# Kernel tuning notes

Measured on AMD Instinct MI355X. Metric: run time of the kernel, lower is better.

## Reference

```python
import jax, jax.numpy as jnp
import numpy as np

HID = 1024
NH = 16
DH = HID // NH  # 64


def _heads(x):
    # [B, S, H] -> [B, nH, S, dh]
    B, S, _ = x.shape
    return x.reshape(B, S, NH, DH).transpose(0, 2, 1, 3)


def setup_inputs() -> dict:
    key = jax.random.key(0)
    ks = jax.random.split(key, 16)
    inp = {
        "word_hidden_states": jax.random.normal(ks[0], (2, 2048, HID), jnp.float32),
        "entity_hidden_states": jax.random.normal(ks[1], (2, 256, HID), jnp.float32),
    }
    scale = 1.0 / np.sqrt(HID)
    names = ["Wq", "Wk", "Wv", "Ww2e", "We2w", "We2e"]
    for i, n in enumerate(names):
        inp[n] = jax.random.normal(ks[2 + i], (HID, HID), jnp.float32) * scale
        inp["b" + n[1:]] = jnp.zeros((HID,), jnp.float32)
    return inp


def reference(word_hidden_states, entity_hidden_states,
              Wq, bq, Wk, bk, Wv, bv,
              Ww2e, bw2e, We2w, be2w, We2e, be2e):
    word, ent = word_hidden_states, entity_hidden_states
    B, Sw, _ = word.shape
    Se = ent.shape[1]
    hs = jnp.concatenate([word, ent], axis=1)  # [B, Sw+Se, H]

    # four query types, heads: [B, nH, S*, dh]
    q_w2w = _heads(word @ Wq + bq)
    q_w2e = _heads(word @ Ww2e + bw2e)
    q_e2w = _heads(ent @ We2w + be2w)
    q_e2e = _heads(ent @ We2e + be2e)

    k = _heads(hs @ Wk + bk)
    v = _heads(hs @ Wv + bv)
    k_w, k_e = k[:, :, :Sw, :], k[:, :, Sw:, :]

    # block scores
    s_w2w = jnp.einsum("bhqd,bhkd->bhqk", q_w2w, k_w)  # [B,nH,Sw,Sw]
    s_w2e = jnp.einsum("bhqd,bhkd->bhqk", q_w2e, k_e)  # [B,nH,Sw,Se]
    s_e2w = jnp.einsum("bhqd,bhkd->bhqk", q_e2w, k_w)  # [B,nH,Se,Sw]
    s_e2e = jnp.einsum("bhqd,bhkd->bhqk", q_e2e, k_e)  # [B,nH,Se,Se]

    word_scores = jnp.concatenate([s_w2w, s_w2e], axis=3)
    ent_scores = jnp.concatenate([s_e2w, s_e2e], axis=3)
    scores = jnp.concatenate([word_scores, ent_scores], axis=2)  # [B,nH,S,S]
    scores = scores / np.sqrt(DH)

    probs = jax.nn.softmax(scores, axis=-1)  # dropout is identity in eval
    ctx = jnp.einsum("bhqk,bhkd->bhqd", probs, v)  # [B,nH,S,dh]
    ctx = ctx.transpose(0, 2, 1, 3).reshape(B, Sw + Se, HID)
    return ctx[:, :Sw, :], ctx[:, Sw:, :]
```

## Files before the change

kernel.cpp:

```cpp
#include <hip/hip_runtime.h>
#include <hip/hip_bf16.h>

typedef __attribute__((ext_vector_type(8))) short short8;
typedef __attribute__((ext_vector_type(4))) float f32x4;
typedef __attribute__((ext_vector_type(16))) float f32x16;
typedef __attribute__((ext_vector_type(4))) unsigned short u16x4;
typedef __attribute__((ext_vector_type(8))) unsigned short u16x8;
typedef __attribute__((ext_vector_type(4))) unsigned int u32x4;

__device__ __forceinline__ unsigned short f2b(float f) {
  __hip_bfloat16 h = __float2bfloat16(f);
  return __builtin_bit_cast(unsigned short, h);
}

__device__ __forceinline__ void gload_lds16(const void* g, void* l) {
  __builtin_amdgcn_global_load_lds(
      (const __attribute__((address_space(1))) unsigned int*)g,
      (__attribute__((address_space(3))) unsigned int*)l, 16, 0, 0);
}

__device__ __forceinline__ f32x16 mfma32(short8 a, short8 b, f32x16 c) {
  return __builtin_amdgcn_mfma_f32_32x32x16_bf16(a, b, c, 0, 0, 0);
}

__device__ __forceinline__ unsigned int cvtpk(float a, float b) {
  unsigned int r;
  asm("v_cvt_pk_bf16_f32 %0, %1, %2" : "=v"(r) : "v"(a), "v"(b));
  return r;
}

__global__ __launch_bounds__(256) void cvt_all(const float* __restrict__ sw,
                                               const float* __restrict__ se,
                                               unsigned short* __restrict__ dw,
                                               unsigned short* __restrict__ de) {
  int i = blockIdx.x * 256 + threadIdx.x;
  const float* s;
  unsigned short* d;
  int j;
  if (i < 524288) {
    s = sw; d = dw; j = i;
  } else {
    s = se; d = de; j = i - 524288;
    if (j >= 65536) return;
  }
  const f32x4* sp = (const f32x4*)s;
  f32x4 a = sp[2 * j];
  f32x4 b = sp[2 * j + 1];
  u16x8 o;
  o[0] = f2b(a[0]); o[1] = f2b(a[1]); o[2] = f2b(a[2]); o[3] = f2b(a[3]);
  o[4] = f2b(b[0]); o[5] = f2b(b[1]); o[6] = f2b(b[2]); o[7] = f2b(b[3]);
  ((u16x8*)d)[j] = o;
}

struct WtransParams {
  const float* w[6];
  unsigned short* wt[6];
};

__global__ __launch_bounds__(256) void wtrans(WtransParams p) {
  __shared__ float t[32][33];
  const int z = blockIdx.z;
  const float* W = p.w[z];
  unsigned short* Wt = p.wt[z];
  const int bx = blockIdx.x;
  const int by = blockIdx.y;
  const int tx = threadIdx.x, ty = threadIdx.y;
#pragma unroll
  for (int i = 0; i < 4; ++i)
    t[ty + 8 * i][tx] = W[(by * 32 + ty + 8 * i) * 1024 + bx * 32 + tx];
  __syncthreads();
#pragma unroll
  for (int i = 0; i < 4; ++i)
    Wt[(bx * 32 + ty + 8 * i) * 1024 + by * 32 + tx] = f2b(t[tx][ty + 8 * i]);
}

struct GemmJob {
  const unsigned short* Wt;
  const float* bias;
  unsigned short* out;
  int S;
  int s_off;
  int sshift;
  int trans;
  float scale;
};
struct Gemm2Params {
  const unsigned short* Aw;
  const unsigned short* Ae;
  GemmJob job[8];
};

__global__ __launch_bounds__(256) void gemm_qkv(Gemm2Params p) {
  __shared__ unsigned short smem[16384];
  unsigned short* As = smem;
  unsigned short* Bs = smem + 8192;
  const int tid = threadIdx.x;
  const int w = tid >> 6, lane = tid & 63;
  const int c = lane & 15, g = lane >> 4;
  const int z = blockIdx.z;
  const int y = blockIdx.y;
  const bool isword = y < 32;
  const GemmJob j = p.job[isword ? z : z + 4];
  const unsigned short* A = isword ? p.Aw : p.Ae;
  const long arow0 = (long)(isword ? y : y - 32) * 128;
  const unsigned short* B = j.Wt;
  const long brow0 = (long)blockIdx.x * 128;

  f32x4 acc[4][4] = {};

  for (int kt = 0; kt < 16; ++kt) {
    __syncthreads();
#pragma unroll
    for (int i = 0; i < 4; ++i) {
      int ch = i * 256 + tid;
      int row = ch >> 3;
      int k8 = ((ch & 7) ^ (row & 7)) << 3;
      const unsigned short* ga = A + (arow0 + row) * 1024 + kt * 64 + k8;
      const unsigned short* gb = B + (brow0 + row) * 1024 + kt * 64 + k8;
      gload_lds16(ga, As + (i * 256 + w * 64) * 8);
      gload_lds16(gb, Bs + (i * 256 + w * 64) * 8);
    }
    __syncthreads();
#pragma unroll
    for (int kf = 0; kf < 2; ++kf) {
      short8 av[4], bv[4];
#pragma unroll
      for (int mf = 0; mf < 4; ++mf) {
        int row = (w >> 1) * 64 + mf * 16 + c;
        int byte = (row * 128 + (kf * 32 + g * 8) * 2) ^ ((row & 7) << 4);
        av[mf] = *(const short8*)((const char*)As + byte);
      }
#pragma unroll
      for (int nf = 0; nf < 4; ++nf) {
        int row = (w & 1) * 64 + nf * 16 + c;
        int byte = (row * 128 + (kf * 32 + g * 8) * 2) ^ ((row & 7) << 4);
        bv[nf] = *(const short8*)((const char*)Bs + byte);
      }
      __builtin_amdgcn_s_setprio(1);
#pragma unroll
      for (int mf = 0; mf < 4; ++mf)
#pragma unroll
        for (int nf = 0; nf < 4; ++nf)
          acc[mf][nf] = __builtin_amdgcn_mfma_f32_16x16x32_bf16(av[mf], bv[nf],
                                                                acc[mf][nf], 0, 0, 0);
      __builtin_amdgcn_s_setprio(0);
    }
  }

  float biasv[4];
#pragma unroll
  for (int nf = 0; nf < 4; ++nf) {
    int n = (int)brow0 + (w & 1) * 64 + nf * 16 + c;
    biasv[nf] = j.bias[n];
  }
  const int smask = (1 << j.sshift) - 1;
  __syncthreads();

  if (j.trans) {
#pragma unroll
    for (int mf = 0; mf < 4; ++mf) {
      int m0 = (w >> 1) * 64 + mf * 16 + g * 4;
#pragma unroll
      for (int nf = 0; nf < 4; ++nf) {
        int n = (w & 1) * 64 + nf * 16 + c;
        u16x4 pv;
#pragma unroll
        for (int r = 0; r < 4; ++r)
          pv[r] = f2b((acc[mf][nf][r] + biasv[nf]) * j.scale);
        int byte = (n * 256 + m0 * 2) ^ ((n & 7) << 4);
        *(u16x4*)((char*)smem + byte) = pv;
      }
    }
    __syncthreads();
#pragma unroll
    for (int i = 0; i < 8; ++i) {
      int ch = i * 256 + tid;
      int nr = ch >> 4, sl = ch & 15;
      int byte = (nr * 256 + sl * 16) ^ ((nr & 7) << 4);
      u16x8 v = *(const u16x8*)((const char*)smem + byte);
      int n = (int)brow0 + nr;
      int hh = n >> 6, dd = n & 63;
      int m = (int)arow0 + sl * 8;
      int b_ = m >> j.sshift;
      int s = (m & smask) + j.s_off;
      *(u16x8*)(j.out + (((long)b_ * 16 + hh) * 64 + dd) * 2304 + s) = v;
    }
  } else {
#pragma unroll
    for (int mf = 0; mf < 4; ++mf) {
#pragma unroll
      for (int r = 0; r < 4; ++r) {
        int m = (w >> 1) * 64 + mf * 16 + g * 4 + r;
#pragma unroll
        for (int nf = 0; nf < 4; ++nf) {
          int n = (w & 1) * 64 + nf * 16 + c;
          unsigned short hv = f2b((acc[mf][nf][r] + biasv[nf]) * j.scale);
          int byte = (m * 256 + n * 2) ^ ((m & 7) << 4);
          *(unsigned short*)((char*)smem + byte) = hv;
        }
      }
    }
    __syncthreads();
#pragma unroll
    for (int i = 0; i < 8; ++i) {
      int ch = i * 256 + tid;
      int mr = ch >> 4, sl = ch & 15;
      int byte = (mr * 256 + sl * 16) ^ ((mr & 7) << 4);
      u16x8 v = *(const u16x8*)((const char*)smem + byte);
      int m = (int)arow0 + mr;
      int b_ = m >> j.sshift;
      int s = (m & smask) + j.s_off;
      int n = (int)brow0 + sl * 8;
      int hh = n >> 6, dd = n & 63;
      *(u16x8*)(j.out + (((long)b_ * 16 + hh) * j.S + s) * 64 + dd) = v;
    }
  }
}

__global__ __launch_bounds__(256) void attn_kernel(
    const unsigned short* __restrict__ qw2w, const unsigned short* __restrict__ qw2e,
    const unsigned short* __restrict__ qe2w, const unsigned short* __restrict__ qe2e,
    const unsigned short* __restrict__ Kg, const unsigned short* __restrict__ Vtg,
    float* __restrict__ po0, float* __restrict__ po1, float* __restrict__ lbuf) {
  __shared__ unsigned short smem[16384];

  const int tid = threadIdx.x;
  const int w = tid >> 6, lane = tid & 63;
  const int l31 = lane & 31, hf = lane >> 5;

  const int flat = blockIdx.x;
  const int work = (flat & 7) * 144 + (flat >> 3);
  const int part = work & 1;
  const int tile = (work % 36) >> 1;
  const int hb = work / 36;
  const int head = hb & 15, b = hb >> 4;

  const bool isw = tile < 16;
  const int Sq = isw ? 2048 : 256;
  const int q0 = (isw ? tile : tile - 16) * 128 + w * 32;
  const int bh = b * 16 + head;
  const unsigned short* Qa =
      (isw ? qw2w : qe2w) + ((long)bh * Sq + q0 + l31) * 64 + hf * 8;
  const unsigned short* Qb =
      (isw ? qw2e : qe2e) + ((long)bh * Sq + q0 + l31) * 64 + hf * 8;
  const unsigned short* Kb = Kg + (long)bh * 2304 * 64;
  const unsigned short* Vtb = Vtg + (long)bh * 64 * 2304;

  short8 qcur[4];
#pragma unroll
  for (int kf = 0; kf < 4; ++kf) qcur[kf] = *(const short8*)(Qa + kf * 16);

  f32x16 o[2] = {};
  float lrun = 0.f;

  auto stage = [&](int t, int bufi) {
    const unsigned short* Kt = Kb + t * 4096;
    unsigned short* Klp = smem + bufi * 4096;
    unsigned short* Vlp = smem + 8192 + bufi * 4096;
#pragma unroll
    for (int i = 0; i < 2; ++i) {
      int ch = i * 256 + tid;
      int row = ch >> 3, c8 = ch & 7;
      int col = (c8 ^ (row & 7)) << 3;
      gload_lds16(Kt + row * 64 + col, Klp + (i * 256 + (tid & 192)) * 8);
      gload_lds16(Vtb + row * 2304 + t * 64 + col, Vlp + (i * 256 + (tid & 192)) * 8);
    }
  };

  const int t0 = part * 18, t1 = t0 + 18;
  stage(t0, 0);
  __syncthreads();
  int cur = 0;

  for (int t = t0; t < t1; ++t) {
    if (t == 32) {
#pragma unroll
      for (int kf = 0; kf < 4; ++kf) qcur[kf] = *(const short8*)(Qb + kf * 16);
    }
    if (t + 1 < t1) stage(t + 1, cur ^ 1);

    const char* Kbase = (const char*)(smem + cur * 4096);
    const char* Vbase = (const char*)(smem + 8192 + cur * 4096);

    f32x16 st[2] = {};
#pragma unroll
    for (int kg = 0; kg < 2; ++kg) {
      int row = kg * 32 + l31;
      int rb = (row * 128) | (hf * 16);
      int sw = (row & 7) << 4;
      short8 kfr[4];
#pragma unroll
      for (int kf = 0; kf < 4; ++kf)
        kfr[kf] = *(const short8*)(Kbase + ((rb + kf * 32) ^ sw));
      __builtin_amdgcn_s_setprio(1);
#pragma unroll
      for (int kf = 0; kf < 4; ++kf) st[kg] = mfma32(kfr[kf], qcur[kf], st[kg]);
      __builtin_amdgcn_s_setprio(0);
    }

    float s0 = 0.f, s1 = 0.f, s2 = 0.f, s3 = 0.f;
#pragma unroll
    for (int kg = 0; kg < 2; ++kg) {
#pragma unroll
      for (int r = 0; r < 16; r += 4) {
        float p0 = __builtin_amdgcn_exp2f(st[kg][r + 0]);
        float p1 = __builtin_amdgcn_exp2f(st[kg][r + 1]);
        float p2 = __builtin_amdgcn_exp2f(st[kg][r + 2]);
        float p3 = __builtin_amdgcn_exp2f(st[kg][r + 3]);
        st[kg][r + 0] = p0; st[kg][r + 1] = p1;
        st[kg][r + 2] = p2; st[kg][r + 3] = p3;
        s0 += p0; s1 += p1; s2 += p2; s3 += p3;
      }
    }
    lrun += (s0 + s1) + (s2 + s3);

#pragma unroll
    for (int kg = 0; kg < 2; ++kg)
#pragma unroll
      for (int hs = 0; hs < 2; ++hs) {
        const int rbase = hs * 8;
        unsigned int a0 = cvtpk(st[kg][rbase + 0], st[kg][rbase + 1]);
        unsigned int a1 = cvtpk(st[kg][rbase + 2], st[kg][rbase + 3]);
        unsigned int b0 = cvtpk(st[kg][rbase + 4], st[kg][rbase + 5]);
        unsigned int b1 = cvtpk(st[kg][rbase + 6], st[kg][rbase + 7]);
        asm("v_permlane32_swap_b32 %0, %1" : "+v"(a0), "+v"(b0));
        asm("v_permlane32_swap_b32 %0, %1" : "+v"(a1), "+v"(b1));
        u32x4 pw;
        pw[0] = a0; pw[1] = a1; pw[2] = b0; pw[3] = b1;
        short8 pf = __builtin_bit_cast(short8, pw);
        const int ks = kg * 2 + hs;
        short8 vf0, vf1;
        {
          int vrow = l31;
          int byte = ((vrow * 128) | (ks * 32 + hf * 16)) ^ ((vrow & 7) << 4);
          vf0 = *(const short8*)(Vbase + byte);
          vrow = 32 + l31;
          byte = ((vrow * 128) | (ks * 32 + hf * 16)) ^ ((vrow & 7) << 4);
          vf1 = *(const short8*)(Vbase + byte);
        }
        __builtin_amdgcn_s_setprio(1);
        o[0] = mfma32(vf0, pf, o[0]);
        o[1] = mfma32(vf1, pf, o[1]);
        __builtin_amdgcn_s_setprio(0);
      }

    __syncthreads();
    cur ^= 1;
  }

  float ltot = lrun + __shfl_xor(lrun, 32);

  const int sgb = (isw ? 0 : 2048) + q0;
  if (hf == 0) lbuf[(long)part * 73728 + bh * 2304 + sgb + l31] = ltot;

  float* E = (float*)smem + w * 2048;
#pragma unroll
  for (int mf = 0; mf < 2; ++mf)
#pragma unroll
    for (int rg = 0; rg < 4; ++rg) {
      int d0 = mf * 32 + rg * 8 + hf * 4;
      f32x4 v;
      v[0] = o[mf][rg * 4 + 0];
      v[1] = o[mf][rg * 4 + 1];
      v[2] = o[mf][rg * 4 + 2];
      v[3] = o[mf][rg * 4 + 3];
      *(f32x4*)(E + l31 * 64 + (d0 ^ ((l31 & 7) << 2))) = v;
    }

  float* po = part ? po1 : po0;
  float* ob = isw ? po + (((long)b * 2048 + q0) * 1024 + head * 64)
                  : po + (long)2 * 2048 * 1024 +
                        (((long)b * 256 + q0) * 1024 + head * 64);
#pragma unroll
  for (int i = 0; i < 8; ++i) {
    int qr = (lane >> 4) + i * 4;
    int dc = (lane & 15) * 4;
    f32x4 v = *(const f32x4*)(E + qr * 64 + (dc ^ ((qr & 7) << 2)));
    *(f32x4*)(ob + (long)qr * 1024 + dc) = v;
  }
}

__global__ __launch_bounds__(256) void attn_merge(const float* __restrict__ po0,
                                                  const float* __restrict__ po1,
                                                  const float* __restrict__ lbuf,
                                                  float* __restrict__ out) {
  long i = ((long)blockIdx.x * 256 + threadIdx.x) * 4;
  if (i >= 4718592) return;
  int bh, sg;
  if (i < 4194304) {
    int b = (int)(i >> 21), s = (int)((i >> 10) & 2047), h = (int)((i >> 6) & 15);
    bh = b * 16 + h;
    sg = s;
  } else {
    long j = i - 4194304;
    int b = (int)(j >> 18), s = (int)((j >> 10) & 255), h = (int)((j >> 6) & 15);
    bh = b * 16 + h;
    sg = 2048 + s;
  }
  float l0 = lbuf[bh * 2304 + sg];
  float l1 = lbuf[73728 + bh * 2304 + sg];
  f32x4 a = *(const f32x4*)(po0 + i);
  f32x4 c = *(const f32x4*)(po1 + i);
  float inv = 1.f / (l0 + l1);
  f32x4 r = (a + c) * inv;
  *(f32x4*)(out + i) = r;
}

extern "C" void kernel_launch(void* const* d_in, const int* in_sizes, int n_in,
                              void* d_out, int out_size, void* d_ws, size_t ws_size,
                              hipStream_t stream) {
  (void)in_sizes; (void)n_in; (void)out_size; (void)ws_size;
  const float* word = (const float*)d_in[0];
  const float* ent = (const float*)d_in[1];

  char* ws = (char*)d_ws;
  size_t off = 0;
  auto alloc = [&](size_t bytes) {
    void* p = ws + off;
    off += (bytes + 255) & ~(size_t)255;
    return p;
  };
  unsigned short* Xw = (unsigned short*)alloc(4096ull * 1024 * 2);
  unsigned short* Xe = (unsigned short*)alloc(512ull * 1024 * 2);
  unsigned short* Wt[6];
  for (int i = 0; i < 6; ++i) Wt[i] = (unsigned short*)alloc(1024ull * 1024 * 2);
  unsigned short* qw2w = (unsigned short*)alloc(2ull * 16 * 2048 * 64 * 2);
  unsigned short* qw2e = (unsigned short*)alloc(2ull * 16 * 2048 * 64 * 2);
  unsigned short* qe2w = (unsigned short*)alloc(2ull * 16 * 256 * 64 * 2);
  unsigned short* qe2e = (unsigned short*)alloc(2ull * 16 * 256 * 64 * 2);
  unsigned short* Kbuf = (unsigned short*)alloc(2ull * 16 * 2304 * 64 * 2);
  unsigned short* Vtbuf = (unsigned short*)alloc(2ull * 16 * 64 * 2304 * 2);
  float* po1 = (float*)alloc(4718592ull * 4);
  float* lbuf = (float*)alloc(2ull * 73728 * 4);
  float* po0 = (float*)ws;

  cvt_all<<<2304, 256, 0, stream>>>(word, ent, Xw, Xe);

  WtransParams wp;
  wp.w[0] = (const float*)d_in[2];
  wp.w[1] = (const float*)d_in[4];
  wp.w[2] = (const float*)d_in[6];
  wp.w[3] = (const float*)d_in[8];
  wp.w[4] = (const float*)d_in[10];
  wp.w[5] = (const float*)d_in[12];
  for (int i = 0; i < 6; ++i) wp.wt[i] = Wt[i];
  wtrans<<<dim3(32, 32, 6), dim3(32, 8), 0, stream>>>(wp);

  const float* bq = (const float*)d_in[3];
  const float* bk = (const float*)d_in[5];
  const float* bv = (const float*)d_in[7];
  const float* bw2e = (const float*)d_in[9];
  const float* be2w = (const float*)d_in[11];
  const float* be2e = (const float*)d_in[13];
  const float qs = 0.125f * 1.44269504f;

  Gemm2Params gp;
  gp.Aw = Xw;
  gp.Ae = Xe;
  gp.job[0] = {Wt[0], bq, qw2w, 2048, 0, 11, 0, qs};
  gp.job[1] = {Wt[3], bw2e, qw2e, 2048, 0, 11, 0, qs};
  gp.job[2] = {Wt[1], bk, Kbuf, 2304, 0, 11, 0, 1.f};
  gp.job[3] = {Wt[2], bv, Vtbuf, 2304, 0, 11, 1, 1.f};
  gp.job[4] = {Wt[4], be2w, qe2w, 256, 0, 8, 0, qs};
  gp.job[5] = {Wt[5], be2e, qe2e, 256, 0, 8, 0, qs};
  gp.job[6] = {Wt[1], bk, Kbuf, 2304, 2048, 8, 0, 1.f};
  gp.job[7] = {Wt[2], bv, Vtbuf, 2304, 2048, 8, 1, 1.f};
  gemm_qkv<<<dim3(8, 36, 4), 256, 0, stream>>>(gp);

  attn_kernel<<<1152, 256, 0, stream>>>(qw2w, qw2e, qe2w, qe2e, Kbuf, Vtbuf,
                                        po0, po1, lbuf);
  attn_merge<<<4608, 256, 0, stream>>>(po0, po1, lbuf, (float*)d_out);
}
```

Measured before the change: 149.3 us.

## Merge conversion and weight-transpose prepasses; relax attention loop barriers with partial vmcnt waits

Folds the activation bf16 conversion kernel and the weight transpose kernel into a single prepass launch, with blocks split by index. This removes one launch and the gap between the two. In the attention loop, the full __syncthreads is replaced by explicit s_waitcnt vmcnt(4) and s_barrier, so the next tile's async global-to-LDS loads can stay in flight while the current tile is consumed. The partial waitcnt relies on the exact count of outstanding loads and risks races if the compiler emits other vector-memory ops.

```diff
diff --git a/kernel.cpp b/kernel.cpp
--- a/kernel.cpp
+++ b/kernel.cpp
@@ -29,49 +29,54 @@
   return r;
 }
 
-__global__ __launch_bounds__(256) void cvt_all(const float* __restrict__ sw,
-                                               const float* __restrict__ se,
-                                               unsigned short* __restrict__ dw,
-                                               unsigned short* __restrict__ de) {
-  int i = blockIdx.x * 256 + threadIdx.x;
-  const float* s;
-  unsigned short* d;
-  int j;
-  if (i < 524288) {
-    s = sw; d = dw; j = i;
-  } else {
-    s = se; d = de; j = i - 524288;
-    if (j >= 65536) return;
-  }
-  const f32x4* sp = (const f32x4*)s;
-  f32x4 a = sp[2 * j];
-  f32x4 b = sp[2 * j + 1];
-  u16x8 o;
-  o[0] = f2b(a[0]); o[1] = f2b(a[1]); o[2] = f2b(a[2]); o[3] = f2b(a[3]);
-  o[4] = f2b(b[0]); o[5] = f2b(b[1]); o[6] = f2b(b[2]); o[7] = f2b(b[3]);
-  ((u16x8*)d)[j] = o;
-}
-
-struct WtransParams {
+struct PrepassParams {
+  const float* sw;
+  const float* se;
+  unsigned short* dw;
+  unsigned short* de;
   const float* w[6];
   unsigned short* wt[6];
 };
 
-__global__ __launch_bounds__(256) void wtrans(WtransParams p) {
-  __shared__ float t[32][33];
-  const int z = blockIdx.z;
-  const float* W = p.w[z];
-  unsigned short* Wt = p.wt[z];
+__global__ __launch_bounds__(256) void prepass(PrepassParams p) {
   const int bx = blockIdx.x;
-  const int by = blockIdx.y;
-  const int tx = threadIdx.x, ty = threadIdx.y;
-#pragma unroll
-  for (int i = 0; i < 4; ++i)
-    t[ty + 8 * i][tx] = W[(by * 32 + ty + 8 * i) * 1024 + bx * 32 + tx];
-  __syncthreads();
-#pragma unroll
-  for (int i = 0; i < 4; ++i)
-    Wt[(bx * 32 + ty + 8 * i) * 1024 + by * 32 + tx] = f2b(t[tx][ty + 8 * i]);
+  const int tid = threadIdx.x;
+  if (bx < 2304) {
+    int i = bx * 256 + tid;
+    const float* s;
+    unsigned short* d;
+    int j;
+    if (i < 524288) {
+      s = p.sw; d = p.dw; j = i;
+    } else {
+      s = p.se; d = p.de; j = i - 524288;
+      if (j >= 65536) return;
+    }
+    const f32x4* sp = (const f32x4*)s;
+    f32x4 a = sp[2 * j];
+    f32x4 b = sp[2 * j + 1];
+    u16x8 o;
+    o[0] = f2b(a[0]); o[1] = f2b(a[1]); o[2] = f2b(a[2]); o[3] = f2b(a[3]);
+    o[4] = f2b(b[0]); o[5] = f2b(b[1]); o[6] = f2b(b[2]); o[7] = f2b(b[3]);
+    ((u16x8*)d)[j] = o;
+  } else {
+    __shared__ float t[32][33];
+    const int idx = bx - 2304;
+    const int z = idx >> 10;
+    const int rem = idx & 1023;
+    const int bxx = rem & 31;
+    const int byy = rem >> 5;
+    const float* W = p.w[z];
+    unsigned short* Wt = p.wt[z];
+    const int tx = tid & 31, ty = tid >> 5;
+#pragma unroll
+    for (int i = 0; i < 4; ++i)
+      t[ty + 8 * i][tx] = W[(byy * 32 + ty + 8 * i) * 1024 + bxx * 32 + tx];
+    __syncthreads();
+#pragma unroll
+    for (int i = 0; i < 4; ++i)
+      Wt[(bxx * 32 + ty + 8 * i) * 1024 + byy * 32 + tx] = f2b(t[tx][ty + 8 * i]);
+  }
 }
 
 struct GemmJob {
@@ -269,7 +274,6 @@
 
   const int t0 = part * 18, t1 = t0 + 18;
   stage(t0, 0);
-  __syncthreads();
   int cur = 0;
 
   for (int t = t0; t < t1; ++t) {
@@ -277,7 +281,14 @@
 #pragma unroll
       for (int kf = 0; kf < 4; ++kf) qcur[kf] = *(const short8*)(Qb + kf * 16);
     }
-    if (t + 1 < t1) stage(t + 1, cur ^ 1);
+    if (t + 1 < t1) {
+      stage(t + 1, cur ^ 1);
+      asm volatile("s_waitcnt vmcnt(4)" ::: "memory");
+    } else {
+      asm volatile("s_waitcnt vmcnt(0)" ::: "memory");
+    }
+    __builtin_amdgcn_sched_barrier(0);
+    __builtin_amdgcn_s_barrier();
 
     const char* Kbase = (const char*)(smem + cur * 4096);
     const char* Vbase = (const char*)(smem + 8192 + cur * 4096);
@@ -344,7 +355,9 @@
         __builtin_amdgcn_s_setprio(0);
       }
 
-    __syncthreads();
+    asm volatile("s_waitcnt lgkmcnt(0)" ::: "memory");
+    __builtin_amdgcn_sched_barrier(0);
+    __builtin_amdgcn_s_barrier();
     cur ^= 1;
   }
 
@@ -434,17 +447,19 @@
   float* lbuf = (float*)alloc(2ull * 73728 * 4);
   float* po0 = (float*)ws;
 
-  cvt_all<<<2304, 256, 0, stream>>>(word, ent, Xw, Xe);
-
-  WtransParams wp;
-  wp.w[0] = (const float*)d_in[2];
-  wp.w[1] = (const float*)d_in[4];
-  wp.w[2] = (const float*)d_in[6];
-  wp.w[3] = (const float*)d_in[8];
-  wp.w[4] = (const float*)d_in[10];
-  wp.w[5] = (const float*)d_in[12];
-  for (int i = 0; i < 6; ++i) wp.wt[i] = Wt[i];
-  wtrans<<<dim3(32, 32, 6), dim3(32, 8), 0, stream>>>(wp);
+  PrepassParams pp;
+  pp.sw = word;
+  pp.se = ent;
+  pp.dw = Xw;
+  pp.de = Xe;
+  pp.w[0] = (const float*)d_in[2];
+  pp.w[1] = (const float*)d_in[4];
+  pp.w[2] = (const float*)d_in[6];
+  pp.w[3] = (const float*)d_in[8];
+  pp.w[4] = (const float*)d_in[10];
+  pp.w[5] = (const float*)d_in[12];
+  for (int i = 0; i < 6; ++i) pp.wt[i] = Wt[i];
+  prepass<<<8448, 256, 0, stream>>>(pp);
 
   const float* bq = (const float*)d_in[3];
   const float* bk = (const float*)d_in[5];
```

Result: no change. 148.1 us (-0.8%).
